# Optimization experiments

Measured on AMD Instinct MI355X. Metric: run time of the kernel, lower is better.

Reference implementation:

```python
import jax, jax.numpy as jnp
import numpy as np
from jax import lax

C = 256        # shared head channels (out_ch)
NB = 6         # anchors per spatial location
NC = 9         # num_classes (incl. background)
B = 16         # batch
FM = [(38, 38), (19, 19), (10, 10), (5, 5), (3, 3), (1, 1)]
BIAS_PRIOR = -float(np.log((1.0 - 0.01) / 0.01))  # focal-style prior on cls bias


def _conv(x, w, b):
    # 3x3 conv, stride 1, SAME padding, NCHW/OIHW
    y = lax.conv_general_dilated(x, w, (1, 1), 'SAME',
                                 dimension_numbers=('NCHW', 'OIHW', 'NCHW'))
    return y + b[None, :, None, None]


def _head(x, ws, bs):
    for w, b in zip(ws[:-1], bs[:-1]):
        x = jax.nn.relu(_conv(x, w, b))
    return _conv(x, ws[-1], bs[-1])


def setup_inputs() -> dict:
    key = jax.random.key(0)
    ks = jax.random.split(key, 20)
    d = {}
    for i, (h, w) in enumerate(FM):
        d[f'feat{i}'] = jax.random.normal(ks[i], (B, C, h, w), dtype=jnp.float32)
    for i in range(4):
        d[f'rw{i}'] = 0.01 * jax.random.normal(ks[6 + i], (C, C, 3, 3), dtype=jnp.float32)
        d[f'rb{i}'] = jnp.zeros((C,), jnp.float32)
    d['rw4'] = 0.01 * jax.random.normal(ks[10], (NB * 4, C, 3, 3), dtype=jnp.float32)
    d['rb4'] = jnp.zeros((NB * 4,), jnp.float32)
    for i in range(4):
        d[f'cw{i}'] = 0.01 * jax.random.normal(ks[11 + i], (C, C, 3, 3), dtype=jnp.float32)
        d[f'cb{i}'] = jnp.zeros((C,), jnp.float32)
    d['cw4'] = 0.01 * jax.random.normal(ks[15], (NB * NC, C, 3, 3), dtype=jnp.float32)
    cb4 = jnp.zeros((NB * NC,), jnp.float32)
    d['cb4'] = cb4.at[:NB].set(BIAS_PRIOR)  # bias_per_class = n_boxes entries
    return d


def reference(feat0, feat1, feat2, feat3, feat4, feat5,
              rw0, rw1, rw2, rw3, rw4, rb0, rb1, rb2, rb3, rb4,
              cw0, cw1, cw2, cw3, cw4, cb0, cb1, cb2, cb3, cb4):
    feats = [feat0, feat1, feat2, feat3, feat4, feat5]
    rws = [rw0, rw1, rw2, rw3, rw4]
    rbs = [rb0, rb1, rb2, rb3, rb4]
    cws = [cw0, cw1, cw2, cw3, cw4]
    cbs = [cb0, cb1, cb2, cb3, cb4]
    locs, confs = [], []
    for x in feats:
        n = x.shape[0]
        locs.append(_head(x, rws, rbs).reshape(n, 4, -1))       # [N,4,NB*H*W]
        confs.append(_head(x, cws, cbs).reshape(n, NC, -1))     # [N,NC,NB*H*W]
    bbox_delta = jnp.concatenate(locs, axis=2)   # [N, 4, total_anchors]
    confidences = jnp.concatenate(confs, axis=2)  # [N, NC, total_anchors]
    return bbox_delta, confidences
```

## Files before the change

### kernel.cpp

```cpp
#include <hip/hip_runtime.h>
#include <hip/hip_bf16.h>

typedef __attribute__((ext_vector_type(8))) __bf16 bf16x8;
typedef __attribute__((ext_vector_type(4))) float f32x4;

__device__ __forceinline__ unsigned short f2bf(float f) {
    unsigned int u = __float_as_uint(f);
    u += 0x7fff + ((u >> 16) & 1);
    return (unsigned short)(u >> 16);
}

__device__ __forceinline__ void gload16(const void* g, void* l) {
    __builtin_amdgcn_global_load_lds(
        (const __attribute__((address_space(1))) void*)g,
        (__attribute__((address_space(3))) void*)l, 16, 0, 0);
}

#define ZOFFB (31040 * 512)

__device__ __forceinline__ void tile256(int rt, int& rb, int& dim, int& row0) {
    if (rt < 91)       { rb = 0;     dim = 38; row0 = rt * 256; }
    else if (rt < 114) { rb = 23104; dim = 19; row0 = (rt - 91) * 256; }
    else if (rt < 121) { rb = 28880; dim = 10; row0 = (rt - 114) * 256; }
    else if (rt < 123) { rb = 30480; dim = 5;  row0 = (rt - 121) * 256; }
    else if (rt < 124) { rb = 30880; dim = 3;  row0 = (rt - 123) * 256; }
    else               { rb = 31024; dim = 1;  row0 = 0; }
    row0 += rb;
}

__device__ __forceinline__ void tile128(int rt, int& rb, int& dim, int& row0, int& aoff) {
    if (rt < 181)      { rb = 0;     dim = 38; row0 = rt * 128;         aoff = 0;     }
    else if (rt < 227) { rb = 23104; dim = 19; row0 = (rt - 181) * 128; aoff = 8664;  }
    else if (rt < 240) { rb = 28880; dim = 10; row0 = (rt - 227) * 128; aoff = 10830; }
    else if (rt < 244) { rb = 30480; dim = 5;  row0 = (rt - 240) * 128; aoff = 11430; }
    else if (rt < 246) { rb = 30880; dim = 3;  row0 = (rt - 244) * 128; aoff = 11580; }
    else               { rb = 31024; dim = 1;  row0 = (rt - 246) * 128; aoff = 11634; }
    row0 += rb;
}

struct WT { const float* src[10]; };
__global__ __launch_bounds__(256) void wtrans_all(WT wt, unsigned short* __restrict__ Wb,
                                                  unsigned short* __restrict__ WF) {
    int cr = blockIdx.x;
    int ci = threadIdx.x;
    const float* src;
    unsigned short* dst;
    int co, Cout;
    if (cr < 2048) {
        int slot = cr >> 8; co = cr & 255;
        src = wt.src[slot];
        dst = Wb + (size_t)slot * 589824 + (size_t)co * 2304;
        Cout = 256;
    } else {
        int r = cr - 2048;
        int slot = r >> 6; co = r & 63;
        src = wt.src[8 + slot];
        dst = WF + (size_t)slot * 147456 + (size_t)co * 2304;
        Cout = slot ? 54 : 24;
    }
    float v[9];
    if (co < Cout) {
        const float* s = src + (size_t)(co * 256 + ci) * 9;
#pragma unroll
        for (int t = 0; t < 9; ++t) v[t] = s[t];
    } else {
#pragma unroll
        for (int t = 0; t < 9; ++t) v[t] = 0.0f;
    }
#pragma unroll
    for (int t = 0; t < 9; ++t) dst[t * 256 + ci] = f2bf(v[t]);
}

struct FT { const float* src[6]; unsigned short* halo[4]; int nh; };
__global__ void ftrans_all(FT ft, unsigned short* __restrict__ X0) {
    int idx = blockIdx.x * 256 + threadIdx.x;
    if (idx >= 993280) {
        int idx2 = idx - 993280;
        int buf = idx2 >> 8, off = idx2 & 255;
        if (buf < ft.nh) ft.halo[buf][off] = 0;
        return;
    }
    int row = idx >> 5;
    int c8  = (idx & 31) << 3;
    int m, rb, dim;
    if (row < 23104)      { m = 0; rb = 0;     dim = 38; }
    else if (row < 28880) { m = 1; rb = 23104; dim = 19; }
    else if (row < 30480) { m = 2; rb = 28880; dim = 10; }
    else if (row < 30880) { m = 3; rb = 30480; dim = 5;  }
    else if (row < 31024) { m = 4; rb = 30880; dim = 3;  }
    else                  { m = 5; rb = 31024; dim = 1;  }
    int HW = dim * dim;
    int rel = row - rb;
    int b = rel / HW;
    int hw = rel - b * HW;
    const float* s = ft.src[m] + (size_t)(b * 256 + c8) * HW + hw;
    union { unsigned short u[8]; uint4 v; } tmp;
#pragma unroll
    for (int j = 0; j < 8; ++j) tmp.u[j] = f2bf(s[(size_t)j * HW]);
    *reinterpret_cast<uint4*>(X0 + ((size_t)row << 8) + c8) = tmp.v;
}

struct GArgs {
    const unsigned short* X[2];
    const unsigned short* W[2];
    const float* B[2];
    unsigned short* Y[2];
};

__global__ __launch_bounds__(512, 2) void conv_gemm(GArgs ga) {
    __shared__ unsigned char As[65536];
    __shared__ unsigned char Bs[65536];

    const int hz = blockIdx.y;
    const unsigned char* __restrict__ Xb = (const unsigned char*)ga.X[hz];
    const unsigned char* __restrict__ Wt = (const unsigned char*)ga.W[hz];
    const float* __restrict__ bias = ga.B[hz];
    unsigned short* __restrict__ Y = ga.Y[hz];

    int rb, dim, row0;
    tile256(blockIdx.x, rb, dim, row0);
    const int HWm = dim * dim;
    const int rowEnd = rb + 16 * HWm;

    const int tid = threadIdx.x;
    const int lane = tid & 63, wid = tid >> 6;
    const int lr = lane & 15, lg = lane >> 4;
    const int wm = wid >> 2, wn = wid & 3;

    const int sr0 = tid >> 2;
    const int xsw = (((tid & 3) ^ ((sr0 >> 1) & 3)) << 4);
    const unsigned char* Zr = Xb + ZOFFB + xsw;

    int gg[2], ay[2], ax[2];
    bool av[2];
#pragma unroll
    for (int it = 0; it < 2; ++it) {
        int g = row0 + sr0 + it * 128;
        bool v = g < rowEnd;
        int rel = v ? (g - rb) : 0;
        int b = rel / HWm;
        int hw = rel - b * HWm;
        int y = hw / dim;
        gg[it] = g; ay[it] = y; ax[it] = hw - y * dim; av[it] = v;
    }

    const unsigned char* bsrc0 = Wt + (size_t)sr0 * 4608 + xsw;
    const unsigned char* bsrc1 = Wt + (size_t)(sr0 + 128) * 4608 + xsw;

    auto tapA = [&](int tap, const unsigned char*& p0, const unsigned char*& p1) {
        int q3 = tap / 3;
        int dy = q3 - 1, dx = tap - q3 * 3 - 1;
        int ddd = dy * dim + dx;
        bool v0 = av[0] && ((unsigned)(ay[0] + dy) < (unsigned)dim) && ((unsigned)(ax[0] + dx) < (unsigned)dim);
        bool v1 = av[1] && ((unsigned)(ay[1] + dy) < (unsigned)dim) && ((unsigned)(ax[1] + dx) < (unsigned)dim);
        p0 = v0 ? Xb + (size_t)(gg[0] + ddd) * 512 + xsw : Zr;
        p1 = v1 ? Xb + (size_t)(gg[1] + ddd) * 512 + xsw : Zr;
    };

    const int fswz = ((lg ^ ((lr >> 1) & 3)) << 4);
    const int aRd = (wm * 128 + lr) * 64 + fswz;
    const int bRd = (wn * 64 + lr) * 64 + fswz;
    const int dSt = wid * 1024;

    f32x4 acc[8][4];
#pragma unroll
    for (int i = 0; i < 8; ++i)
#pragma unroll
        for (int j = 0; j < 4; ++j) acc[i][j] = (f32x4){0.f, 0.f, 0.f, 0.f};

    const unsigned char *aC0, *aC1, *aN0, *aN1;
    tapA(0, aC0, aC1);
#pragma unroll
    for (int kt = 0; kt < 3; ++kt) {
        gload16(aC0 + kt * 64, As + kt * 16384 + dSt);
        gload16(aC1 + kt * 64, As + kt * 16384 + 8192 + dSt);
        gload16(bsrc0 + kt * 64, Bs + kt * 16384 + dSt);
        gload16(bsrc1 + kt * 64, Bs + kt * 16384 + 8192 + dSt);
    }

#pragma unroll 1
    for (int tap = 0; tap < 9; ++tap) {
        if (tap < 8) tapA(tap + 1, aN0, aN1);
        else { aN0 = Zr; aN1 = Zr; }
        const unsigned char* bT0 = bsrc0 + tap * 512;
        const unsigned char* bT1 = bsrc1 + tap * 512;

#pragma unroll
        for (int kc = 0; kc < 8; ++kc) {
            const int bufc = kc & 3;
            const int bufs = (kc + 3) & 3;

            asm volatile("s_waitcnt vmcnt(8)" ::: "memory");
            __builtin_amdgcn_s_barrier();
            asm volatile("" ::: "memory");

            {
                const unsigned char *sa0, *sa1, *sb0, *sb1;
                if (kc < 5) {
                    sa0 = aC0 + (kc + 3) * 64; sa1 = aC1 + (kc + 3) * 64;
                    sb0 = bT0 + (kc + 3) * 64; sb1 = bT1 + (kc + 3) * 64;
                } else {
                    sa0 = aN0 + (kc - 5) * 64; sa1 = aN1 + (kc - 5) * 64;
                    sb0 = bT0 + 512 + (kc - 5) * 64; sb1 = bT1 + 512 + (kc - 5) * 64;
                }
                gload16(sa0, As + bufs * 16384 + dSt);
                gload16(sa1, As + bufs * 16384 + 8192 + dSt);
                gload16(sb0, Bs + bufs * 16384 + dSt);
                gload16(sb1, Bs + bufs * 16384 + 8192 + dSt);
            }

            const unsigned char* ab = As + bufc * 16384;
            const unsigned char* bb = Bs + bufc * 16384;
            bf16x8 rA[8], rB[4];
#pragma unroll
            for (int j = 0; j < 4; ++j) rB[j] = *(const bf16x8*)(bb + bRd + j * 1024);
#pragma unroll
            for (int i = 0; i < 8; ++i) rA[i] = *(const bf16x8*)(ab + aRd + i * 1024);
#pragma unroll
            for (int i = 0; i < 8; ++i)
#pragma unroll
                for (int j = 0; j < 4; ++j)
                    acc[i][j] = __builtin_amdgcn_mfma_f32_16x16x32_bf16(rA[i], rB[j], acc[i][j], 0, 0, 0);
        }
        aC0 = aN0; aC1 = aN1;
    }

    float bj[4];
#pragma unroll
    for (int j = 0; j < 4; ++j) bj[j] = bias[wn * 64 + j * 16 + lr];
#pragma unroll
    for (int i = 0; i < 8; ++i) {
        int rbase = row0 + wm * 128 + i * 16 + lg * 4;
#pragma unroll
        for (int rr = 0; rr < 4; ++rr) {
            int orow = rbase + rr;
            if (orow < rowEnd) {
                size_t yb = (size_t)orow * 256 + wn * 64 + lr;
#pragma unroll
                for (int j = 0; j < 4; ++j) {
                    float v = acc[i][j][rr] + bj[j];
                    Y[yb + j * 16] = f2bf(fmaxf(v, 0.f));
                }
            }
        }
    }
}

struct FArgs {
    const unsigned short* X[2];
    const unsigned short* W[2];
    const float* B[2];
    float* out;
    int hbase;
};

__global__ __launch_bounds__(256) void conv_final(FArgs fa) {
    __shared__ unsigned char As[2][8192];
    __shared__ unsigned char Bs[2][4096];

    const int zi = blockIdx.z;
    const int hz = zi + fa.hbase;
    const unsigned char* Xb = (const unsigned char*)fa.X[zi];
    const unsigned char* Wt = (const unsigned char*)fa.W[zi];
    const float* bias = fa.B[zi];
    float* out = fa.out;

    int rb, dim, row0, aoff;
    tile128(blockIdx.x, rb, dim, row0, aoff);
    const int HWm = dim * dim;
    const int rowEnd = rb + 16 * HWm;

    const int tid = threadIdx.x;
    const int lane = tid & 63, wid = tid >> 6;
    const int lr = lane & 15, lg = lane >> 4;

    const int swz16 = (((lane & 3) ^ ((lane >> 3) & 3)) << 4);
    const int srow = wid * 16 + (lane >> 2);

    int ay[2], ax[2], arel[2];
    bool av0[2];
#pragma unroll
    for (int it = 0; it < 2; ++it) {
        int r = row0 + it * 64 + srow;
        bool v = r < rowEnd;
        int rel = v ? (r - rb) : 0;
        int b = rel / HWm;
        int hw = rel - b * HWm;
        int y = hw / dim;
        ay[it] = y; ax[it] = hw - y * dim; arel[it] = rel; av0[it] = v;
    }

    const unsigned char* bB = Wt + (size_t)srow * 4608 + swz16;

    const int fsw = ((lg ^ ((lr >> 1) & 3)) << 4);
    const int aRd = (wid * 32 + lr) * 64 + fsw;
    const int bRd = lr * 64 + fsw;
    const int dA0 = wid * 1024;

    f32x4 acc[2][4];
#pragma unroll
    for (int i = 0; i < 2; ++i)
#pragma unroll
        for (int j = 0; j < 4; ++j) acc[i][j] = (f32x4){0.f, 0.f, 0.f, 0.f};

    auto tapPtr = [&](int tap, const unsigned char** aP) {
        int q3 = tap / 3;
        int dy = q3 - 1, dx = tap - q3 * 3 - 1;
#pragma unroll
        for (int it = 0; it < 2; ++it) {
            bool v = av0[it] && ((unsigned)(ay[it] + dy) < (unsigned)dim)
                             && ((unsigned)(ax[it] + dx) < (unsigned)dim);
            int off = v ? (rb + arel[it] + dy * dim + dx) * 512 : ZOFFB;
            aP[it] = Xb + off + swz16;
        }
    };

    const unsigned char* aP[2];
    tapPtr(0, aP);
    gload16(aP[0], &As[0][dA0]);
    gload16(aP[1], &As[0][dA0 + 4096]);
    gload16(bB, &Bs[0][dA0]);
    __syncthreads();

#pragma unroll 1
    for (int tap = 0; tap < 9; ++tap) {
        const unsigned char* aPn[2];
        if (tap < 8) tapPtr(tap + 1, aPn);
        else { aPn[0] = aP[0]; aPn[1] = aP[1]; }
        const unsigned char* bP = bB + tap * 512;

#pragma unroll
        for (int kin = 0; kin < 8; ++kin) {
            const int cur = kin & 1, nxt = cur ^ 1;
            if (kin < 7) {
                gload16(aP[0] + (kin + 1) * 64, &As[nxt][dA0]);
                gload16(aP[1] + (kin + 1) * 64, &As[nxt][dA0 + 4096]);
                gload16(bP + (kin + 1) * 64, &Bs[nxt][dA0]);
            } else if (tap < 8) {
                gload16(aPn[0], &As[nxt][dA0]);
                gload16(aPn[1], &As[nxt][dA0 + 4096]);
                gload16(bP + 512, &Bs[nxt][dA0]);
            }
            bf16x8 af[2], bg[4];
#pragma unroll
            for (int i = 0; i < 2; ++i)
                af[i] = *(const bf16x8*)(&As[cur][0] + aRd + i * 1024);
#pragma unroll
            for (int j = 0; j < 4; ++j)
                bg[j] = *(const bf16x8*)(&Bs[cur][0] + bRd + j * 1024);
#pragma unroll
            for (int i = 0; i < 2; ++i)
#pragma unroll
                for (int j = 0; j < 4; ++j)
                    acc[i][j] = __builtin_amdgcn_mfma_f32_16x16x32_bf16(af[i], bg[j], acc[i][j], 0, 0, 0);
            __syncthreads();
        }
        aP[0] = aPn[0]; aP[1] = aPn[1];
    }

    const int Cout = hz ? 54 : 24;
#pragma unroll
    for (int i = 0; i < 2; ++i) {
        int rbase = row0 + wid * 32 + i * 16 + lg * 4;
#pragma unroll
        for (int r = 0; r < 4; ++r) {
            int orow = rbase + r;
            if (orow < rowEnd) {
                int rel = orow - rb;
                int b = rel / HWm;
                int hw = rel - b * HWm;
#pragma unroll
                for (int j = 0; j < 4; ++j) {
                    int oc = j * 16 + lr;
                    if (oc < Cout) {
                        int q = oc / 6;
                        int s = oc - q * 6;
                        int anchor = aoff + s * HWm + hw;
                        float v = acc[i][j][r] + bias[oc];
                        if (hz)
                            out[744960 + (size_t)b * 104760 + (size_t)q * 11640 + anchor] = v;
                        else
                            out[(size_t)b * 46560 + (size_t)q * 11640 + anchor] = v;
                    }
                }
            }
        }
    }
}

extern "C" void kernel_launch(void* const* d_in, const int* in_sizes, int n_in,
                              void* d_out, int out_size, void* d_ws, size_t ws_size,
                              hipStream_t stream) {
    (void)in_sizes; (void)n_in; (void)out_size;

    const float* rw[5]  = {(const float*)d_in[6],  (const float*)d_in[8],
                           (const float*)d_in[10], (const float*)d_in[12],
                           (const float*)d_in[14]};
    const float* rbv[5] = {(const float*)d_in[7],  (const float*)d_in[9],
                           (const float*)d_in[11], (const float*)d_in[13],
                           (const float*)d_in[15]};
    const float* cw[5]  = {(const float*)d_in[16], (const float*)d_in[18],
                           (const float*)d_in[20], (const float*)d_in[22],
                           (const float*)d_in[24]};
    const float* cbv[5] = {(const float*)d_in[17], (const float*)d_in[19],
                           (const float*)d_in[21], (const float*)d_in[23],
                           (const float*)d_in[25]};

    const size_t ACTB = 31041ull * 512;
    const size_t WMAT = 589824;
    const size_t WBYTES = 8 * WMAT * 2;
    const size_t WFBYTES = 2 * 147456 * 2;
    const size_t needF = 4 * ACTB + WBYTES + WFBYTES;
    const size_t needS = 3 * ACTB + WBYTES + WFBYTES;

    unsigned char* ws = (unsigned char*)d_ws;
    bool fused = (ws_size >= needF);
    if (!fused && ws_size < needS) return;

    int nact = fused ? 4 : 3;
    unsigned short* act[4];
    for (int i = 0; i < nact; ++i) act[i] = (unsigned short*)(ws + (size_t)i * ACTB);
    unsigned short* Wb = (unsigned short*)(ws + (size_t)nact * ACTB);
    unsigned short* WF = (unsigned short*)(ws + (size_t)nact * ACTB + WBYTES);

    WT wt;
    for (int l = 0; l < 4; ++l) { wt.src[l] = rw[l]; wt.src[4 + l] = cw[l]; }
    wt.src[8] = rw[4]; wt.src[9] = cw[4];
    wtrans_all<<<2176, 256, 0, stream>>>(wt, Wb, WF);

    FT ft;
    for (int i = 0; i < 6; ++i) ft.src[i] = (const float*)d_in[i];
    for (int i = 0; i < 4; ++i)
        ft.halo[i] = (unsigned short*)((unsigned char*)act[i < nact ? i : 0] + ZOFFB);
    ft.nh = nact;
    ftrans_all<<<3884, 256, 0, stream>>>(ft, act[0]);

    const unsigned short* Wr[5], *Wc[5];
    for (int l = 0; l < 4; ++l) {
        Wr[l] = Wb + (size_t)l * WMAT;
        Wc[l] = Wb + (size_t)(4 + l) * WMAT;
    }
    Wr[4] = WF; Wc[4] = WF + 147456;

    if (fused) {
        unsigned short* X0 = act[0];
        unsigned short* P = act[1];
        unsigned short* Q = act[2];
        unsigned short* R = act[3];
        GArgs l1 = {{X0, X0}, {Wr[0], Wc[0]}, {rbv[0], cbv[0]}, {P, Q}};
        GArgs l2 = {{P,  Q},  {Wr[1], Wc[1]}, {rbv[1], cbv[1]}, {X0, R}};
        GArgs l3 = {{X0, R},  {Wr[2], Wc[2]}, {rbv[2], cbv[2]}, {P, Q}};
        GArgs l4 = {{P,  Q},  {Wr[3], Wc[3]}, {rbv[3], cbv[3]}, {X0, R}};
        conv_gemm<<<dim3(125, 2), 512, 0, stream>>>(l1);
        conv_gemm<<<dim3(125, 2), 512, 0, stream>>>(l2);
        conv_gemm<<<dim3(125, 2), 512, 0, stream>>>(l3);
        conv_gemm<<<dim3(125, 2), 512, 0, stream>>>(l4);
        FArgs lf = {{X0, R}, {Wr[4], Wc[4]}, {rbv[4], cbv[4]}, (float*)d_out, 0};
        conv_final<<<dim3(247, 1, 2), 256, 0, stream>>>(lf);
    } else {
        unsigned short* X0 = act[0];
        unsigned short* A1 = act[1];
        unsigned short* A2 = act[2];
        for (int h = 0; h < 2; ++h) {
            const unsigned short* const* W = h ? Wc : Wr;
            const float* const* bs = h ? cbv : rbv;
            GArgs l1 = {{X0, X0}, {W[0], W[0]}, {bs[0], bs[0]}, {A1, A1}};
            GArgs l2 = {{A1, A1}, {W[1], W[1]}, {bs[1], bs[1]}, {A2, A2}};
            GArgs l3 = {{A2, A2}, {W[2], W[2]}, {bs[2], bs[2]}, {A1, A1}};
            GArgs l4 = {{A1, A1}, {W[3], W[3]}, {bs[3], bs[3]}, {A2, A2}};
            conv_gemm<<<dim3(125, 1), 512, 0, stream>>>(l1);
            conv_gemm<<<dim3(125, 1), 512, 0, stream>>>(l2);
            conv_gemm<<<dim3(125, 1), 512, 0, stream>>>(l3);
            conv_gemm<<<dim3(125, 1), 512, 0, stream>>>(l4);
            FArgs lf = {{A2, A2}, {W[4], W[4]}, {bs[4], bs[4]}, (float*)d_out, h};
            conv_final<<<dim3(247, 1, 1), 256, 0, stream>>>(lf);
        }
    }
}
```

Baseline: 376.8 us.

## Deepen conv_final LDS pipeline to four stages with vmcnt-based waits

Replaces the double-buffered LDS staging in the final head conv kernel with a 4-slot ring buffer that keeps three K-slices in flight. It uses an explicit s_waitcnt vmcnt(6) plus a raw barrier in place of a full __syncthreads after each MFMA step. The goal is to hide global-load latency behind the MFMAs. In exchange it raises LDS use to 48KB per block, which may reduce occupancy, and it issues dummy loads from a zero row at the tail to keep the wait counts uniform.

```diff
diff --git a/kernel.cpp b/kernel.cpp
--- a/kernel.cpp
+++ b/kernel.cpp
@@ -255,8 +255,8 @@
 };
 
 __global__ __launch_bounds__(256) void conv_final(FArgs fa) {
-    __shared__ unsigned char As[2][8192];
-    __shared__ unsigned char Bs[2][4096];
+    __shared__ unsigned char As[32768];
+    __shared__ unsigned char Bs[16384];
 
     const int zi = blockIdx.z;
     const int hz = zi + fa.hbase;
@@ -276,6 +276,7 @@
 
     const int swz16 = (((lane & 3) ^ ((lane >> 3) & 3)) << 4);
     const int srow = wid * 16 + (lane >> 2);
+    const unsigned char* Zr = Xb + ZOFFB + swz16;
 
     int ay[2], ax[2], arel[2];
     bool av0[2];
@@ -316,44 +317,57 @@
     };
 
     const unsigned char* aP[2];
+    const unsigned char* aPn[2];
     tapPtr(0, aP);
-    gload16(aP[0], &As[0][dA0]);
-    gload16(aP[1], &As[0][dA0 + 4096]);
-    gload16(bB, &Bs[0][dA0]);
-    __syncthreads();
+#pragma unroll
+    for (int kt = 0; kt < 3; ++kt) {
+        gload16(aP[0] + kt * 64, As + kt * 8192 + dA0);
+        gload16(aP[1] + kt * 64, As + kt * 8192 + 4096 + dA0);
+        gload16(bB + kt * 64, Bs + kt * 4096 + dA0);
+    }
 
 #pragma unroll 1
     for (int tap = 0; tap < 9; ++tap) {
-        const unsigned char* aPn[2];
         if (tap < 8) tapPtr(tap + 1, aPn);
-        else { aPn[0] = aP[0]; aPn[1] = aP[1]; }
+        else { aPn[0] = Zr; aPn[1] = Zr; }
         const unsigned char* bP = bB + tap * 512;
 
 #pragma unroll
         for (int kin = 0; kin < 8; ++kin) {
-            const int cur = kin & 1, nxt = cur ^ 1;
-            if (kin < 7) {
-                gload16(aP[0] + (kin + 1) * 64, &As[nxt][dA0]);
-                gload16(aP[1] + (kin + 1) * 64, &As[nxt][dA0 + 4096]);
-                gload16(bP + (kin + 1) * 64, &Bs[nxt][dA0]);
-            } else if (tap < 8) {
-                gload16(aPn[0], &As[nxt][dA0]);
-                gload16(aPn[1], &As[nxt][dA0 + 4096]);
-                gload16(bP + 512, &Bs[nxt][dA0]);
+            const int sc = kin & 3;
+            const int ss = (kin + 3) & 3;
+
+            asm volatile("s_waitcnt vmcnt(6)" ::: "memory");
+            __builtin_amdgcn_s_barrier();
+            asm volatile("" ::: "memory");
+
+            {
+                const unsigned char *sa0, *sa1, *sb;
+                if (tap == 8 && kin >= 5) { sa0 = Zr; sa1 = Zr; sb = Zr; }
+                else if (kin < 5) {
+                    sa0 = aP[0] + (kin + 3) * 64; sa1 = aP[1] + (kin + 3) * 64;
+                    sb = bP + (kin + 3) * 64;
+                } else {
+                    sa0 = aPn[0] + (kin - 5) * 64; sa1 = aPn[1] + (kin - 5) * 64;
+                    sb = bP + 512 + (kin - 5) * 64;
+                }
+                gload16(sa0, As + ss * 8192 + dA0);
+                gload16(sa1, As + ss * 8192 + 4096 + dA0);
+                gload16(sb, Bs + ss * 4096 + dA0);
             }
+
+            const unsigned char* ab = As + sc * 8192;
+            const unsigned char* bb = Bs + sc * 4096;
             bf16x8 af[2], bg[4];
 #pragma unroll
-            for (int i = 0; i < 2; ++i)
-                af[i] = *(const bf16x8*)(&As[cur][0] + aRd + i * 1024);
-#pragma unroll
-            for (int j = 0; j < 4; ++j)
-                bg[j] = *(const bf16x8*)(&Bs[cur][0] + bRd + j * 1024);
+            for (int j = 0; j < 4; ++j) bg[j] = *(const bf16x8*)(bb + bRd + j * 1024);
+#pragma unroll
+            for (int i = 0; i < 2; ++i) af[i] = *(const bf16x8*)(ab + aRd + i * 1024);
 #pragma unroll
             for (int i = 0; i < 2; ++i)
 #pragma unroll
                 for (int j = 0; j < 4; ++j)
                     acc[i][j] = __builtin_amdgcn_mfma_f32_16x16x32_bf16(af[i], bg[j], acc[i][j], 0, 0, 0);
-            __syncthreads();
         }
         aP[0] = aPn[0]; aP[1] = aPn[1];
     }
```

Measured after the change: 373.4 us, median of 3. Within noise of the previous version (-0.9%).
